# Performance work log

Measured on AMD Instinct MI355X. Metric: run time of the kernel, lower is better.

## Reference

```python
import jax, jax.numpy as jnp
import numpy as np
from jax import lax

B, N, C = 4, 8000, 91
IMG_H, IMG_W = 800, 1333
WX, WY, WW, WH = 10.0, 10.0, 5.0, 5.0
BBOX_XFORM_CLIP = float(np.log(1000.0 / 16.0))
SCORE_THRESH = 0.05
NMS_THRESH = 0.5
DET_PER_IMG = 100
MIN_SIZE = 0.01
NEG = jnp.float32(-1e30)


def setup_inputs() -> dict:
    key = jax.random.key(0)
    k1, k2, k3 = jax.random.split(key, 3)
    class_logits = jax.random.normal(k1, (B * N, C), dtype=jnp.float32) * 2.0
    box_regression = jax.random.normal(k2, (B * N, C * 4), dtype=jnp.float32) * 0.5
    p = jax.random.uniform(k3, (B, N, 4), dtype=jnp.float32)
    x1 = p[..., 0] * (IMG_W - 150.0)
    y1 = p[..., 1] * (IMG_H - 150.0)
    x2 = x1 + 4.0 + p[..., 2] * 140.0
    y2 = y1 + 4.0 + p[..., 3] * 140.0
    proposals = jnp.stack([x1, y1, x2, y2], axis=-1)
    return {"class_logits": class_logits, "box_regression": box_regression, "proposals": proposals}


def _decode(rel, props):
    # torchvision BoxCoder.decode with weights (10,10,5,5). rel: [N, C*4], props: [N, 4]
    w = props[:, 2] - props[:, 0]
    h = props[:, 3] - props[:, 1]
    cx = props[:, 0] + 0.5 * w
    cy = props[:, 1] + 0.5 * h
    rel = rel.reshape(rel.shape[0], -1, 4)  # [N, C, 4]
    dx = rel[..., 0] / WX
    dy = rel[..., 1] / WY
    dw = jnp.minimum(rel[..., 2] / WW, BBOX_XFORM_CLIP)
    dh = jnp.minimum(rel[..., 3] / WH, BBOX_XFORM_CLIP)
    pcx = dx * w[:, None] + cx[:, None]
    pcy = dy * h[:, None] + cy[:, None]
    pw = jnp.exp(dw) * w[:, None]
    ph = jnp.exp(dh) * h[:, None]
    return jnp.stack([pcx - 0.5 * pw, pcy - 0.5 * ph, pcx + 0.5 * pw, pcy + 0.5 * ph], axis=-1)


def _iou_one_vs_all(b, bs):
    # b: [4], bs: [M, 4]
    ix1 = jnp.maximum(b[0], bs[:, 0])
    iy1 = jnp.maximum(b[1], bs[:, 1])
    ix2 = jnp.minimum(b[2], bs[:, 2])
    iy2 = jnp.minimum(b[3], bs[:, 3])
    inter = jnp.clip(ix2 - ix1, 0.0) * jnp.clip(iy2 - iy1, 0.0)
    a1 = (b[2] - b[0]) * (b[3] - b[1])
    a2 = (bs[:, 2] - bs[:, 0]) * (bs[:, 3] - bs[:, 1])
    return inter / (a1 + a2 - inter)


def _process_image(logits, rel, props):
    # logits: [N, C], rel: [N, C*4], props: [N, 4]
    boxes = _decode(rel, props)  # [N, C, 4]
    # clip_boxes_to_image
    boxes = jnp.stack([
        jnp.clip(boxes[..., 0], 0.0, IMG_W),
        jnp.clip(boxes[..., 1], 0.0, IMG_H),
        jnp.clip(boxes[..., 2], 0.0, IMG_W),
        jnp.clip(boxes[..., 3], 0.0, IMG_H),
    ], axis=-1)
    scores = jax.nn.softmax(logits, axis=-1)
    # drop background class 0 and flatten to [N*(C-1)] candidates
    boxes = boxes[:, 1:, :].reshape(-1, 4)
    scores = scores[:, 1:].reshape(-1)
    labels = jnp.broadcast_to(jnp.arange(1, C, dtype=jnp.int32), (N, C - 1)).reshape(-1)
    bw = boxes[:, 2] - boxes[:, 0]
    bh = boxes[:, 3] - boxes[:, 1]
    valid = (scores > SCORE_THRESH) & (bw >= MIN_SIZE) & (bh >= MIN_SIZE)
    # batched_nms: offset boxes per class so cross-class boxes never overlap
    sg_boxes = lax.stop_gradient(boxes)
    sg_scores = lax.stop_gradient(jnp.where(valid, scores, NEG))
    off = labels.astype(boxes.dtype) * (sg_boxes.max() + 1.0)
    nb = sg_boxes + off[:, None]

    def step(s, _):
        i = jnp.argmax(s)
        si = s[i]
        iou = _iou_one_vs_all(nb[i], nb)
        s2 = jnp.where(iou > NMS_THRESH, NEG, s).at[i].set(NEG)
        return s2, (i, si > NEG / 2)

    _, (idxs, ok) = lax.scan(step, sg_scores, None, length=DET_PER_IMG)
    det_boxes = jnp.where(ok[:, None], boxes[idxs], 0.0)
    det_scores = jnp.where(ok, scores[idxs], 0.0)
    det_labels = jnp.where(ok, labels[idxs], 0)
    return det_boxes, det_scores, det_labels


def reference(class_logits, box_regression, proposals):
    logits = class_logits.reshape(B, N, C)
    rel = box_regression.reshape(B, N, C * 4)
    boxes, scores, labels = jax.vmap(_process_image)(logits, rel, proposals)
    return boxes, scores, labels
```

## Files before the change

### kernel.cpp

```cpp
#include <hip/hip_runtime.h>
#include <math.h>

#pragma clang fp contract(off)

#define NB 4
#define NN 8000
#define NC 91
#define CM1 90
#define CAP 2048
#define ACAP 256
#define ATHR 192
#define GCAP 65536
#define RPB 32
#define BPI (NN / RPB)
#define LCAP 608
#define GWB 16

#define CNT_W(b) ((b) * 64)
#define MAX_W(b) (256 + (b) * 64)
#define CNTA_W(b) (512 + (b) * 64)
#define CNTR_W(b) (768 + (b) * 64)
#define HIST_OFF 1024
#define ZERO_WORDS (HIST_OFF + NB * 1024)
#define GBOX_OFF 5120
#define GSC_OFF (GBOX_OFF + NB * GCAP * 4)
#define GOID_OFF (GSC_OFF + NB * GCAP)
#define ABOX_OFF (GOID_OFF + NB * GCAP)
#define AKEY_OFF (ABOX_OFF + NB * ACAP * 4)
#define RBOX_OFF (AKEY_OFF + NB * ACAP * 2)
#define RKEY_OFF (RBOX_OFF + NB * CAP * 4)

__global__ void init_kernel(int* ws_i) {
  const int i = blockIdx.x * 256 + threadIdx.x;
  if (i < ZERO_WORDS) ws_i[i] = 0;
}

__global__ void __launch_bounds__(256) cand_kernel(const float* __restrict__ logits,
                                                   const float* __restrict__ rel,
                                                   const float* __restrict__ props,
                                                   int* __restrict__ ws_i,
                                                   float* __restrict__ ws_f) {
  const int blk = blockIdx.x;
  const int b = blk / BPI;
  const int ib = blk - b * BPI;
  const int t = threadIdx.x;
  const int L = t & 15;
  const int grp = t >> 4;
  const int lane = t & 63;

  __shared__ float sbx[LCAP][4];
  __shared__ float ssb[LCAP];
  __shared__ int soidb[LCAP];
  __shared__ int lhist[1024];
  __shared__ int scnt;
  __shared__ int smaxs;
  __shared__ int sgbase;
  for (int j = t; j < 1024; j += 256) lhist[j] = 0;
  if (t == 0) { scnt = 0; smaxs = 0; }
  __syncthreads();

  int tmax = 0;

  for (int i = 0; i < RPB / 16; ++i) {
    const int row = b * NN + ib * RPB + i * 16 + grp;
    const float* lp = logits + (size_t)row * NC;

    float lv[6];
#pragma unroll
    for (int j = 0; j < 6; ++j) {
      const int k = L + 16 * j;
      lv[j] = (k < NC) ? lp[k] : -INFINITY;
    }
    float tm0 = fmax(lv[0], lv[4]), tm1 = fmax(lv[1], lv[5]);
    float tm2 = lv[2], tm3 = lv[3];
    float um0 = fmax(tm0, tm2), um1 = fmax(tm1, tm3);
    float m = fmax(um0, um1);
    m = fmaxf(m, __shfl_xor(m, 8));
    m = fmaxf(m, __shfl_xor(m, 4));
    m = fmaxf(m, __shfl_xor(m, 2));
    m = fmaxf(m, __shfl_xor(m, 1));

    float ev[6];
#pragma unroll
    for (int j = 0; j < 6; ++j) {
      const int k = L + 16 * j;
      ev[j] = (k < NC) ? expf(lv[j] - m) : 0.0f;
    }
    float ts0 = ev[0] + ev[4], ts1 = ev[1] + ev[5];
    float ts2 = ev[2], ts3 = ev[3];
    float us0 = ts0 + ts2, us1 = ts1 + ts3;
    float sum = us0 + us1;
    sum += __shfl_xor(sum, 8);
    sum += __shfl_xor(sum, 4);
    sum += __shfl_xor(sum, 2);
    sum += __shfl_xor(sum, 1);

    const float4 p = reinterpret_cast<const float4*>(props)[row];
    const float w = p.z - p.x, h = p.w - p.y;
    const float cx = p.x + 0.5f * w, cy = p.y + 0.5f * h;

#pragma unroll
    for (int j = 0; j < 6; ++j) {
      const int c = L + 16 * j;
      if (c >= 1 && c < NC) {
        const float4 r = reinterpret_cast<const float4*>(rel)[(size_t)row * NC + c];
        const float dx = r.x / 10.0f, dy = r.y / 10.0f;
        const float dw = fminf(r.z / 5.0f, 4.135166556742356f);
        const float dh = fminf(r.w / 5.0f, 4.135166556742356f);
        const float pcx = dx * w + cx, pcy = dy * h + cy;
        const float pw = expf(dw) * w, ph = expf(dh) * h;
        float x1 = pcx - 0.5f * pw, y1 = pcy - 0.5f * ph;
        float x2 = pcx + 0.5f * pw, y2 = pcy + 0.5f * ph;
        x1 = fminf(fmaxf(x1, 0.0f), 1333.0f);
        y1 = fminf(fmaxf(y1, 0.0f), 800.0f);
        x2 = fminf(fmaxf(x2, 0.0f), 1333.0f);
        y2 = fminf(fmaxf(y2, 0.0f), 800.0f);
        const float score = ev[j] / sum;
        const float localmax = fmaxf(fmaxf(x1, y1), fmaxf(x2, y2));
        tmax = max(tmax, __float_as_int(localmax));
        const float bw = x2 - x1, bh = y2 - y1;
        if ((score > 0.05f) && (bw >= 0.01f) && (bh >= 0.01f)) {
          const int slot = atomicAdd(&scnt, 1);
          sbx[slot][0] = x1; sbx[slot][1] = y1;
          sbx[slot][2] = x2; sbx[slot][3] = y2;
          ssb[slot] = score;
          soidb[slot] = (row - b * NN) * CM1 + (c - 1);
          int bi = (int)(__float_as_uint(score) >> 16) - 15360;
          bi = min(max(bi, 0), 1023);
          atomicAdd(&lhist[bi], 1);
        }
      }
    }
  }
  tmax = max(tmax, __shfl_xor(tmax, 32));
  tmax = max(tmax, __shfl_xor(tmax, 16));
  tmax = max(tmax, __shfl_xor(tmax, 8));
  tmax = max(tmax, __shfl_xor(tmax, 4));
  tmax = max(tmax, __shfl_xor(tmax, 2));
  tmax = max(tmax, __shfl_xor(tmax, 1));
  if (lane == 0) atomicMax(&smaxs, tmax);
  __syncthreads();
  const int n = scnt;
  if (t == 0) {
    sgbase = atomicAdd(&ws_i[CNT_W(b)], n);
    atomicMax(&ws_i[MAX_W(b)], smaxs);
  }
  __syncthreads();
  const int gb = sgbase;
  for (int j = t; j < n; j += 256) {
    const int pos = gb + j;
    if (pos < GCAP) {
      reinterpret_cast<float4*>(ws_f + GBOX_OFF)[b * GCAP + pos] =
          make_float4(sbx[j][0], sbx[j][1], sbx[j][2], sbx[j][3]);
      ws_f[GSC_OFF + b * GCAP + pos] = ssb[j];
      ws_i[GOID_OFF + b * GCAP + pos] = soidb[j];
    }
  }
  for (int j = t; j < 1024; j += 256) {
    const int v = lhist[j];
    if (v) atomicAdd(&ws_i[HIST_OFF + b * 1024 + j], v);
  }
}

__global__ void __launch_bounds__(256) gather_kernel(int* __restrict__ ws_i,
                                                     float* __restrict__ ws_f) {
  const int b = blockIdx.x / GWB, sub = blockIdx.x % GWB;
  const int t = threadIdx.x;
  __shared__ int seg[256];
  __shared__ int best1, best2;
  __shared__ int lidxA[ACAP];
  __shared__ int lidxR[CAP];
  __shared__ int cA, cR, baseA, baseR;

  const int* H = ws_i + HIST_OFF + b * 1024;
  const int h0 = H[4 * t + 0], h1 = H[4 * t + 1];
  const int h2 = H[4 * t + 2], h3 = H[4 * t + 3];
  seg[t] = h0 + h1 + h2 + h3;
  if (t == 0) { best1 = 1024; best2 = 1024; cA = 0; cR = 0; }
  __syncthreads();
  for (int off = 1; off < 256; off <<= 1) {
    const int v = (t + off < 256) ? seg[t + off] : 0;
    __syncthreads();
    seg[t] += v;
    __syncthreads();
  }
  const int higher = (t < 255) ? seg[t + 1] : 0;
  {
    int A = higher; int cnd = 0x7FFFFFFF;
    A += h3; if (A <= CAP) cnd = 4 * t + 3;
    A += h2; if (A <= CAP) cnd = 4 * t + 2;
    A += h1; if (A <= CAP) cnd = 4 * t + 1;
    A += h0; if (A <= CAP) cnd = 4 * t + 0;
    if (cnd != 0x7FFFFFFF) atomicMin(&best1, cnd);
  }
  {
    int A = higher; int cnd = 0x7FFFFFFF;
    A += h3; if (A <= ATHR) cnd = 4 * t + 3;
    A += h2; if (A <= ATHR) cnd = 4 * t + 2;
    A += h1; if (A <= ATHR) cnd = 4 * t + 1;
    A += h0; if (A <= ATHR) cnd = 4 * t + 0;
    if (cnd != 0x7FFFFFFF) atomicMin(&best2, cnd);
  }
  __syncthreads();
  const int tk = best1, tk2 = best2;

  int M = ws_i[CNT_W(b)];
  if (M > GCAP) M = GCAP;
  const float* gsc = ws_f + GSC_OFF + (size_t)b * GCAP;
  const int* goid = ws_i + GOID_OFF + (size_t)b * GCAP;
  const float4* gbox = reinterpret_cast<const float4*>(ws_f + GBOX_OFF) + (size_t)b * GCAP;
  float4* abox = reinterpret_cast<float4*>(ws_f + ABOX_OFF) + (size_t)b * ACAP;
  unsigned long long* akey = reinterpret_cast<unsigned long long*>(ws_i + AKEY_OFF) + (size_t)b * ACAP;
  float4* rbox = reinterpret_cast<float4*>(ws_f + RBOX_OFF) + (size_t)b * CAP;
  unsigned long long* rkey = reinterpret_cast<unsigned long long*>(ws_i + RKEY_OFF) + (size_t)b * CAP;

  for (int j = sub * 256 + t; j < M; j += GWB * 256) {
    const float s = gsc[j];
    int bi = (int)(__float_as_uint(s) >> 16) - 15360;
    bi = min(max(bi, 0), 1023);
    if (bi >= tk2) {
      const int p = atomicAdd(&cA, 1);
      if (p < ACAP) lidxA[p] = j;
    } else if (bi >= tk) {
      const int p = atomicAdd(&cR, 1);
      if (p < CAP) lidxR[p] = j;
    }
  }
  __syncthreads();
  const int nAb = min(cA, ACAP), nRb = min(cR, CAP);
  if (t == 0) {
    baseA = atomicAdd(&ws_i[CNTA_W(b)], nAb);
    baseR = atomicAdd(&ws_i[CNTR_W(b)], nRb);
  }
  __syncthreads();
  for (int k = t; k < nAb; k += 256) {
    const int j = lidxA[k];
    const int pos = baseA + k;
    if (pos < ACAP) {
      abox[pos] = gbox[j];
      akey[pos] = ((unsigned long long)(__float_as_uint(gsc[j]) | 0x80000000u) << 32) |
                  (unsigned)(0xFFFFFFFFu - (unsigned)goid[j]);
    }
  }
  for (int k = t; k < nRb; k += 256) {
    const int j = lidxR[k];
    const int pos = baseR + k;
    if (pos < CAP) {
      rbox[pos] = gbox[j];
      rkey[pos] = ((unsigned long long)(__float_as_uint(gsc[j]) | 0x80000000u) << 32) |
                  (unsigned)(0xFFFFFFFFu - (unsigned)goid[j]);
    }
  }
}

__global__ void __launch_bounds__(256) nms_kernel(const int* __restrict__ ws_i,
                                                  const float* __restrict__ ws_f,
                                                  float* __restrict__ out) {
  const int b = blockIdx.x;
  const int t = threadIdx.x;
  const int lane = t & 63;
  __shared__ __align__(16) char sm[57344];
  unsigned long long* akey = (unsigned long long*)sm;
  float4* abox = (float4*)(sm + 2048);
  unsigned long long* skeyS = (unsigned long long*)(sm + 6144);
  float4* sboxS = (float4*)(sm + 8192);
  int* slblS = (int*)(sm + 12288);
  unsigned long long* rkeyS = (unsigned long long*)sm;
  float4* rboxS = (float4*)(sm + 16384);
  int* rlblS = (int*)(sm + 49152);
  __shared__ float4 selbox[100];
  __shared__ unsigned long long selkey[100];
  __shared__ int sellbl[100];
  __shared__ int snacc;
  __shared__ int sneed;

  const int nA = min(ws_i[CNTA_W(b)], ACAP);
  const int nR = min(ws_i[CNTR_W(b)], CAP);
  const float maxp1 = __int_as_float(ws_i[MAX_W(b)]) + 1.0f;
  const float4* gA = reinterpret_cast<const float4*>(ws_f + ABOX_OFF) + (size_t)b * ACAP;
  const unsigned long long* gAk =
      reinterpret_cast<const unsigned long long*>(ws_i + AKEY_OFF) + (size_t)b * ACAP;

  akey[t] = (t < nA) ? gAk[t] : 0ull;
  if (t < nA) abox[t] = gA[t];
  skeyS[t] = 0ull;
  __syncthreads();

  {
    const unsigned long long kj = akey[t];
    if (kj != 0ull) {
      int rank = 0;
#pragma unroll 16
      for (int i = 0; i < ACAP; ++i) rank += (akey[i] > kj) ? 1 : 0;
      skeyS[rank] = kj;
      sboxS[rank] = abox[t];
      const unsigned oid = 0xFFFFFFFFu - (unsigned)(kj & 0xFFFFFFFFull);
      slblS[rank] = (int)(oid % 90u) + 1;
    }
  }
  __syncthreads();

  float A0x = 0.f, A0y = 0.f, A0z = 0.f, A0w = 0.f; int L0 = -1;
  float A1x = 0.f, A1y = 0.f, A1z = 0.f, A1w = 0.f; int L1 = -1;
  int nacc = 0;

  if (t < 64) {
    unsigned long long k0 = skeyS[0], k1 = skeyS[1];
    float4 b0 = sboxS[0], b1 = sboxS[1];
    int l0 = slblS[0], l1 = slblS[1];
    for (int j = 0; j < ACAP; ++j) {
      if (k0 == 0ull) break;
      const int jp = j + 2;
      unsigned long long k2 = 0ull;
      float4 b2 = make_float4(0.f, 0.f, 0.f, 0.f);
      int l2 = 0;
      if (jp < ACAP) { k2 = skeyS[jp]; b2 = sboxS[jp]; l2 = slblS[jp]; }
      const float oi = (float)l0 * maxp1;
      const float q0 = b0.x + oi, q1 = b0.y + oi;
      const float q2 = b0.z + oi, q3 = b0.w + oi;
      const float a2 = (q2 - q0) * (q3 - q1);
      bool sup = false;
      if (L0 == l0) {
        const float n0 = A0x + oi, n1 = A0y + oi, n2 = A0z + oi, n3 = A0w + oi;
        const float a1 = (n2 - n0) * (n3 - n1);
        const float ix1 = fmaxf(n0, q0), iy1 = fmaxf(n1, q1);
        const float ix2 = fminf(n2, q2), iy2 = fminf(n3, q3);
        const float inter = fmaxf(ix2 - ix1, 0.0f) * fmaxf(iy2 - iy1, 0.0f);
        const float iou = inter / ((a1 + a2) - inter);
        sup = (iou > 0.5f);
      }
      if (L1 == l0) {
        const float n0 = A1x + oi, n1 = A1y + oi, n2 = A1z + oi, n3 = A1w + oi;
        const float a1 = (n2 - n0) * (n3 - n1);
        const float ix1 = fmaxf(n0, q0), iy1 = fmaxf(n1, q1);
        const float ix2 = fminf(n2, q2), iy2 = fminf(n3, q3);
        const float inter = fmaxf(ix2 - ix1, 0.0f) * fmaxf(iy2 - iy1, 0.0f);
        const float iou = inter / ((a1 + a2) - inter);
        sup = sup || (iou > 0.5f);
      }
      if (!__any(sup ? 1 : 0)) {
        if (nacc < 64) {
          if (lane == nacc) { A0x = b0.x; A0y = b0.y; A0z = b0.z; A0w = b0.w; L0 = l0; }
        } else {
          if (lane == nacc - 64) { A1x = b0.x; A1y = b0.y; A1z = b0.z; A1w = b0.w; L1 = l0; }
        }
        if (lane == 0) { selbox[nacc] = b0; selkey[nacc] = k0; sellbl[nacc] = l0; }
        ++nacc;
        if (nacc == 100) break;
      }
      k0 = k1; b0 = b1; l0 = l1;
      k1 = k2; b1 = b2; l1 = l2;
    }
    if (lane == 0) { snacc = nacc; sneed = (nacc < 100 && nR > 0) ? 1 : 0; }
  }
  __syncthreads();

  if (sneed) {
    const float4* gR = reinterpret_cast<const float4*>(ws_f + RBOX_OFF) + (size_t)b * CAP;
    const unsigned long long* gRk =
        reinterpret_cast<const unsigned long long*>(ws_i + RKEY_OFF) + (size_t)b * CAP;
    for (int j = t; j < CAP; j += 256) {
      const unsigned long long k = (j < nR) ? gRk[j] : 0ull;
      rkeyS[j] = k;
      if (j < nR) {
        rboxS[j] = gR[j];
        const unsigned oid = 0xFFFFFFFFu - (unsigned)(k & 0xFFFFFFFFull);
        rlblS[j] = (int)(oid % 90u) + 1;
      }
    }
    __syncthreads();
    if (t < 64) {
      while (nacc < 100) {
        unsigned long long mk = 0ull; int mi = 0;
        for (int j = lane; j < nR; j += 64) {
          const unsigned long long k = rkeyS[j];
          if (k > mk) { mk = k; mi = j; }
        }
        for (int mm = 1; mm < 64; mm <<= 1) {
          const unsigned long long ok = __shfl_xor(mk, mm);
          const int om = __shfl_xor(mi, mm);
          if (ok > mk) { mk = ok; mi = om; }
        }
        if (mk == 0ull) break;
        if (lane == 0) rkeyS[mi] = 0ull;
        __asm__ volatile("s_waitcnt lgkmcnt(0)" ::: "memory");
        const int lbl = rlblS[mi];
        const float4 bb = rboxS[mi];
        const float oi = (float)lbl * maxp1;
        const float q0 = bb.x + oi, q1 = bb.y + oi;
        const float q2 = bb.z + oi, q3 = bb.w + oi;
        const float a2 = (q2 - q0) * (q3 - q1);
        bool sup = false;
        if (L0 == lbl) {
          const float n0 = A0x + oi, n1 = A0y + oi, n2 = A0z + oi, n3 = A0w + oi;
          const float a1 = (n2 - n0) * (n3 - n1);
          const float ix1 = fmaxf(n0, q0), iy1 = fmaxf(n1, q1);
          const float ix2 = fminf(n2, q2), iy2 = fminf(n3, q3);
          const float inter = fmaxf(ix2 - ix1, 0.0f) * fmaxf(iy2 - iy1, 0.0f);
          const float iou = inter / ((a1 + a2) - inter);
          sup = (iou > 0.5f);
        }
        if (L1 == lbl) {
          const float n0 = A1x + oi, n1 = A1y + oi, n2 = A1z + oi, n3 = A1w + oi;
          const float a1 = (n2 - n0) * (n3 - n1);
          const float ix1 = fmaxf(n0, q0), iy1 = fmaxf(n1, q1);
          const float ix2 = fminf(n2, q2), iy2 = fminf(n3, q3);
          const float inter = fmaxf(ix2 - ix1, 0.0f) * fmaxf(iy2 - iy1, 0.0f);
          const float iou = inter / ((a1 + a2) - inter);
          sup = sup || (iou > 0.5f);
        }
        if (!__any(sup ? 1 : 0)) {
          if (nacc < 64) {
            if (lane == nacc) { A0x = bb.x; A0y = bb.y; A0z = bb.z; A0w = bb.w; L0 = lbl; }
          } else {
            if (lane == nacc - 64) { A1x = bb.x; A1y = bb.y; A1z = bb.z; A1w = bb.w; L1 = lbl; }
          }
          if (lane == 0) { selbox[nacc] = bb; selkey[nacc] = mk; sellbl[nacc] = lbl; }
          ++nacc;
        }
      }
      if (lane == 0) snacc = nacc;
    }
    __syncthreads();
  }

  const int nf = snacc;
  for (int k2 = t; k2 < 100; k2 += 256) {
    float o0 = 0.f, o1 = 0.f, o2 = 0.f, o3 = 0.f, sc = 0.f, lb = 0.f;
    if (k2 < nf) {
      const float4 v = selbox[k2];
      o0 = v.x; o1 = v.y; o2 = v.z; o3 = v.w;
      sc = __uint_as_float((unsigned)(selkey[k2] >> 32) & 0x7FFFFFFFu);
      lb = (float)sellbl[k2];
    }
    float* ob = out + ((size_t)b * 100 + k2) * 4;
    ob[0] = o0; ob[1] = o1; ob[2] = o2; ob[3] = o3;
    out[NB * 100 * 4 + b * 100 + k2] = sc;
    out[NB * 100 * 4 + NB * 100 + b * 100 + k2] = lb;
  }
}

extern "C" void kernel_launch(void* const* d_in, const int* in_sizes, int n_in,
                              void* d_out, int out_size, void* d_ws, size_t ws_size,
                              hipStream_t stream) {
  const float* logits = (const float*)d_in[0];
  const float* rel = (const float*)d_in[1];
  const float* props = (const float*)d_in[2];
  float* out = (float*)d_out;
  int* ws_i = (int*)d_ws;
  float* ws_f = (float*)d_ws;

  init_kernel<<<(ZERO_WORDS + 255) / 256, 256, 0, stream>>>(ws_i);
  cand_kernel<<<NB * BPI, 256, 0, stream>>>(logits, rel, props, ws_i, ws_f);
  gather_kernel<<<NB * GWB, 256, 0, stream>>>(ws_i, ws_f);
  nms_kernel<<<NB, 256, 0, stream>>>(ws_i, ws_f, out);
}
```

Measured before the change: 81.65 us.

## Precompute pairwise suppression bitmask for top candidates and scan it in parallel

Before the serial greedy NMS loop, each thread computes IoU of its sorted candidate against all later same-class candidates and stores a 256-bit suppression mask in shared memory. Every thread then redundantly scans the masks to perform greedy selection, and if 100 detections are reached (or there is no remainder set), it writes the outputs directly and returns early. This replaces the wavefront-serial per-candidate IoU check with parallel O(n^2) mask construction followed by a cheap bitwise scan. The cost is extra shared-memory use and quadratic work with per-thread imbalance, since thread i loops over n-i candidates.

```diff
diff --git a/kernel.cpp b/kernel.cpp
--- a/kernel.cpp
+++ b/kernel.cpp
@@ -265,6 +265,7 @@
   unsigned long long* skeyS = (unsigned long long*)(sm + 6144);
   float4* sboxS = (float4*)(sm + 8192);
   int* slblS = (int*)(sm + 12288);
+  unsigned long long* suppm = (unsigned long long*)(sm + 13312);
   unsigned long long* rkeyS = (unsigned long long*)sm;
   float4* rboxS = (float4*)(sm + 16384);
   int* rlblS = (int*)(sm + 49152);
@@ -272,7 +273,6 @@
   __shared__ unsigned long long selkey[100];
   __shared__ int sellbl[100];
   __shared__ int snacc;
-  __shared__ int sneed;
 
   const int nA = min(ws_i[CNTA_W(b)], ACAP);
   const int nR = min(ws_i[CNTR_W(b)], CAP);
@@ -299,6 +299,83 @@
     }
   }
   __syncthreads();
+
+  {
+    const int i = t;
+    unsigned long long r0 = 0, r1 = 0, r2 = 0, r3 = 0;
+    if (i < nA) {
+      const int li = slblS[i];
+      const float4 bi = sboxS[i];
+      const float oi = (float)li * maxp1;
+      const float n0 = bi.x + oi, n1 = bi.y + oi;
+      const float n2 = bi.z + oi, n3 = bi.w + oi;
+      const float a1 = (n2 - n0) * (n3 - n1);
+      for (int j = i + 1; j < nA; ++j) {
+        if (slblS[j] == li) {
+          const float4 bj = sboxS[j];
+          const float q0 = bj.x + oi, q1 = bj.y + oi;
+          const float q2 = bj.z + oi, q3 = bj.w + oi;
+          const float ix1 = fmaxf(n0, q0), iy1 = fmaxf(n1, q1);
+          const float ix2 = fminf(n2, q2), iy2 = fminf(n3, q3);
+          const float inter = fmaxf(ix2 - ix1, 0.0f) * fmaxf(iy2 - iy1, 0.0f);
+          const float a2 = (q2 - q0) * (q3 - q1);
+          const float iou = inter / ((a1 + a2) - inter);
+          if (iou > 0.5f) {
+            if (j < 64) r0 |= 1ull << j;
+            else if (j < 128) r1 |= 1ull << (j - 64);
+            else if (j < 192) r2 |= 1ull << (j - 128);
+            else r3 |= 1ull << (j - 192);
+          }
+        }
+      }
+    }
+    suppm[i * 4 + 0] = r0; suppm[i * 4 + 1] = r1;
+    suppm[i * 4 + 2] = r2; suppm[i * 4 + 3] = r3;
+  }
+  __syncthreads();
+
+  unsigned long long m0 = 0, m1 = 0, m2 = 0, m3 = 0;
+  int cnt = 0;
+  int mypos = -1;
+#define NMS_CHUNK(W, MW)                                              \
+  if (cnt < 100) {                                                    \
+    for (int jj = 0; jj < 64; ++jj) {                                 \
+      const int j = (W) * 64 + jj;                                    \
+      if (j >= nA || cnt == 100) break;                               \
+      const unsigned long long s0 = suppm[j * 4 + 0];                 \
+      const unsigned long long s1 = suppm[j * 4 + 1];                 \
+      const unsigned long long s2 = suppm[j * 4 + 2];                 \
+      const unsigned long long s3 = suppm[j * 4 + 3];                 \
+      if (!((MW >> jj) & 1ull)) {                                     \
+        if (cnt == t) mypos = j;                                      \
+        ++cnt;                                                        \
+        m0 |= s0; m1 |= s1; m2 |= s2; m3 |= s3;                       \
+      }                                                               \
+    }                                                                 \
+  }
+  NMS_CHUNK(0, m0)
+  NMS_CHUNK(1, m1)
+  NMS_CHUNK(2, m2)
+  NMS_CHUNK(3, m3)
+#undef NMS_CHUNK
+
+  if (cnt >= 100 || nR == 0) {
+    const int nf = min(cnt, 100);
+    if (t < 100) {
+      float o0 = 0.f, o1 = 0.f, o2 = 0.f, o3 = 0.f, sc = 0.f, lb = 0.f;
+      if (t < nf) {
+        const float4 v = sboxS[mypos];
+        o0 = v.x; o1 = v.y; o2 = v.z; o3 = v.w;
+        sc = __uint_as_float((unsigned)(skeyS[mypos] >> 32) & 0x7FFFFFFFu);
+        lb = (float)slblS[mypos];
+      }
+      float* ob = out + ((size_t)b * 100 + t) * 4;
+      ob[0] = o0; ob[1] = o1; ob[2] = o2; ob[3] = o3;
+      out[NB * 100 * 4 + b * 100 + t] = sc;
+      out[NB * 100 * 4 + NB * 100 + b * 100 + t] = lb;
+    }
+    return;
+  }
 
   float A0x = 0.f, A0y = 0.f, A0z = 0.f, A0w = 0.f; int L0 = -1;
   float A1x = 0.f, A1y = 0.f, A1z = 0.f, A1w = 0.f; int L1 = -1;
@@ -351,11 +428,11 @@
       k0 = k1; b0 = b1; l0 = l1;
       k1 = k2; b1 = b2; l1 = l2;
     }
-    if (lane == 0) { snacc = nacc; sneed = (nacc < 100 && nR > 0) ? 1 : 0; }
-  }
-  __syncthreads();
-
-  if (sneed) {
+    if (lane == 0) snacc = nacc;
+  }
+  __syncthreads();
+
+  if (snacc < 100 && nR > 0) {
     const float4* gR = reinterpret_cast<const float4*>(ws_f + RBOX_OFF) + (size_t)b * CAP;
     const unsigned long long* gRk =
         reinterpret_cast<const unsigned long long*>(ws_i + RKEY_OFF) + (size_t)b * CAP;
```

Result: no change. 82.50 us (+1.0%).
